# Kernel tuning notes

Hardware: AMD Instinct MI355X
Metric: run time of the kernel (lower is better)

The kernel has to match this reference:

```python
import jax, jax.numpy as jnp
import numpy as np

N = 100000      # nodes
E = 1600000     # edges
G = 256         # graphs in the batch
D_IN = 128
H = 128
C = 10
EPS = 1e-5      # BatchNorm eps


def setup_inputs() -> dict:
    key = jax.random.key(0)
    ks = jax.random.split(key, 32)
    inp = {
        'x': jax.random.normal(ks[0], (N, D_IN), jnp.float32),
        'edge_index': jax.random.randint(ks[1], (2, E), 0, N, dtype=jnp.int64),
        'batch': jnp.sort(jax.random.randint(ks[2], (N,), 0, G, dtype=jnp.int64)),
        'w1': jax.random.normal(ks[3], (D_IN, H), jnp.float32) * 0.05,
        'b1': jax.random.normal(ks[4], (H,), jnp.float32) * 0.05,
        'w2': jax.random.normal(ks[5], (H, H), jnp.float32) * 0.05,
        'b2': jax.random.normal(ks[6], (H,), jnp.float32) * 0.05,
        'w3': jax.random.normal(ks[7], (H, H), jnp.float32) * 0.05,
        'b3': jax.random.normal(ks[8], (H,), jnp.float32) * 0.05,
        'g1': jax.random.uniform(ks[9], (H,), jnp.float32, 0.5, 1.5),
        'be1': jax.random.normal(ks[10], (H,), jnp.float32) * 0.05,
        'm1': jax.random.normal(ks[11], (H,), jnp.float32) * 0.05,
        'v1': jax.random.uniform(ks[12], (H,), jnp.float32, 0.5, 1.5),
        'g2': jax.random.uniform(ks[13], (H,), jnp.float32, 0.5, 1.5),
        'be2': jax.random.normal(ks[14], (H,), jnp.float32) * 0.05,
        'm2': jax.random.normal(ks[15], (H,), jnp.float32) * 0.05,
        'v2': jax.random.uniform(ks[16], (H,), jnp.float32, 0.5, 1.5),
        'g3': jax.random.uniform(ks[17], (H,), jnp.float32, 0.5, 1.5),
        'be3': jax.random.normal(ks[18], (H,), jnp.float32) * 0.05,
        'm3': jax.random.normal(ks[19], (H,), jnp.float32) * 0.05,
        'v3': jax.random.uniform(ks[20], (H,), jnp.float32, 0.5, 1.5),
        'fcw1': jax.random.normal(ks[21], (H, H // 2), jnp.float32) * 0.05,
        'fcb1': jax.random.normal(ks[22], (H // 2,), jnp.float32) * 0.05,
        'fcw2': jax.random.normal(ks[23], (H // 2, C), jnp.float32) * 0.05,
        'fcb2': jax.random.normal(ks[24], (C,), jnp.float32) * 0.05,
    }
    return inp


def _gcn_norm(edge_index, n_nodes):
    # add self loops (PyG GCNConv default) and compute D^-1/2 (A+I) D^-1/2 norms
    loop = jnp.arange(n_nodes, dtype=edge_index.dtype)
    src = jnp.concatenate([edge_index[0], loop])
    dst = jnp.concatenate([edge_index[1], loop])
    deg = jax.ops.segment_sum(jnp.ones_like(dst, dtype=jnp.float32), dst, num_segments=n_nodes)
    dinv = jnp.where(deg > 0, jax.lax.rsqrt(deg), 0.0)
    norm = dinv[src] * dinv[dst]  # [E+N]
    return src, dst, norm


def _gcn_conv(x, W, b, src, dst, norm, n_nodes):
    h = x @ W                                   # [N, H]
    msg = norm[:, None] * h[src]                # gather + scale, [E+N, H]
    return jax.ops.segment_sum(msg, dst, num_segments=n_nodes) + b


def _bn_eval(x, gamma, beta, mean, var):
    return (x - mean) * jax.lax.rsqrt(var + EPS) * gamma + beta


def reference(x, edge_index, batch, w1, b1, w2, b2, w3, b3,
              g1, be1, m1, v1, g2, be2, m2, v2, g3, be3, m3, v3,
              fcw1, fcb1, fcw2, fcb2):
    n = x.shape[0]
    x = jnp.nan_to_num(x, nan=0.0, posinf=1e6, neginf=-1e6)
    src, dst, norm = _gcn_norm(edge_index, n)

    h = jax.nn.relu(_bn_eval(_gcn_conv(x, w1, b1, src, dst, norm, n), g1, be1, m1, v1))
    h = jax.nn.relu(_bn_eval(_gcn_conv(h, w2, b2, src, dst, norm, n), g2, be2, m2, v2))
    h = jax.nn.relu(_bn_eval(_gcn_conv(h, w3, b3, src, dst, norm, n), g3, be3, m3, v3))

    # global_mean_pool over graphs
    sums = jax.ops.segment_sum(h, batch, num_segments=G)            # [G, H]
    cnts = jax.ops.segment_sum(jnp.ones((n,), h.dtype), batch, num_segments=G)
    pooled = sums / jnp.maximum(cnts, 1.0)[:, None]

    out = jax.nn.relu(pooled @ fcw1 + fcb1) @ fcw2 + fcb2           # [G, C]
    return out
```

## Files before the change

### kernel.cpp

```cpp
#include <hip/hip_runtime.h>
#include <math.h>

#define NN 100000
#define EE 1600000
#define GG 256
#define HH 128
#define BSH 8
#define NBK 391
#define PASSA_WG 391
#define CAPB 6144

typedef __attribute__((ext_vector_type(8))) short short8;
typedef __attribute__((ext_vector_type(4))) float f32x4;

union U4S8 { uint4 u; short8 s; };

static __device__ __forceinline__ unsigned bf16rne(float f) {
    const unsigned u = __float_as_uint(f);
    return (u + 0x7fffu + ((u >> 16) & 1u)) >> 16;
}
static __device__ __forceinline__ unsigned packbf(float a, float b) {
    return bf16rne(a) | (bf16rne(b) << 16);
}
static __device__ __forceinline__ float bflo(unsigned u) { return __uint_as_float(u << 16); }
static __device__ __forceinline__ float bfhi(unsigned u) { return __uint_as_float(u & 0xffff0000u); }

__global__ void detect_k(const int* __restrict__ ei, const int* __restrict__ batch,
                         int* __restrict__ flags) {
    if (threadIdx.x == 0 && blockIdx.x == 0) {
        int e64 = 1;
        for (int j = 0; j < 8; ++j) {
            if (ei[2 * EE - 1 - 2 * j] != 0) { e64 = 0; break; }
        }
        flags[0] = e64;
        flags[1] = (batch[NN - 1] == 0) ? 1 : 0;
    }
}

__global__ __launch_bounds__(512) void cursinit_k(int* __restrict__ cursor) {
    const int b = blockIdx.x * 512 + threadIdx.x;
    if (b < NBK) cursor[b] = b * CAPB;
}

__global__ void bnprep_k(const float* __restrict__ b1, const float* __restrict__ g1,
                         const float* __restrict__ be1, const float* __restrict__ m1,
                         const float* __restrict__ v1,
                         const float* __restrict__ b2, const float* __restrict__ g2,
                         const float* __restrict__ be2, const float* __restrict__ m2,
                         const float* __restrict__ v2,
                         const float* __restrict__ b3, const float* __restrict__ g3,
                         const float* __restrict__ be3, const float* __restrict__ m3,
                         const float* __restrict__ v3,
                         float* __restrict__ sc, float* __restrict__ sh) {
    const int c = threadIdx.x;
    float s;
    s = g1[c] / sqrtf(v1[c] + 1e-5f);
    sc[c] = s;           sh[c] = (b1[c] - m1[c]) * s + be1[c];
    s = g2[c] / sqrtf(v2[c] + 1e-5f);
    sc[128 + c] = s;     sh[128 + c] = (b2[c] - m2[c]) * s + be2[c];
    s = g3[c] / sqrtf(v3[c] + 1e-5f);
    sc[256 + c] = s;     sh[256 + c] = (b3[c] - m3[c]) * s + be3[c];
}

__global__ __launch_bounds__(256) void wprep_k(const float* __restrict__ w1,
                                               const float* __restrict__ w2,
                                               const float* __restrict__ w3,
                                               unsigned* __restrict__ bt) {
    const int id = blockIdx.x * 256 + threadIdx.x;
    if (id >= 3 * 8192) return;
    const int w = id >> 13;
    const int rem = id & 8191;
    const int n = rem >> 6;
    const int kk = rem & 63;
    const float* W = (w == 0) ? w1 : (w == 1) ? w2 : w3;
    bt[id] = packbf(W[(2 * kk) * HH + n], W[(2 * kk + 1) * HH + n]);
}

__global__ __launch_bounds__(256) void passA_k(const int* __restrict__ ei,
                                               const int* __restrict__ flags,
                                               int* __restrict__ cursor,
                                               unsigned* __restrict__ pairs) {
    __shared__ int h[NBK];
    __shared__ int rbase[NBK];
    const int tid = threadIdx.x;
    for (int i = tid; i < NBK; i += 256) h[i] = 0;
    __syncthreads();
    const bool e64 = flags[0] != 0;
    const int base = blockIdx.x * 4096;
    int scache[16], dcache[16];
#pragma unroll
    for (int j = 0; j < 16; ++j) {
        const int e = base + j * 256 + tid;
        int s = -1, d = 0;
        if (e < EE) {
            s = e64 ? ei[2 * e] : ei[e];
            d = e64 ? ei[2 * (EE + e)] : ei[EE + e];
            atomicAdd(&h[d >> BSH], 1);
        }
        scache[j] = s; dcache[j] = d;
    }
    __syncthreads();
    for (int i = tid; i < NBK; i += 256) {
        const int c = h[i];
        rbase[i] = c ? atomicAdd(&cursor[i], c) : 0;
    }
    __syncthreads();
    for (int i = tid; i < NBK; i += 256) h[i] = 0;
    __syncthreads();
#pragma unroll
    for (int j = 0; j < 16; ++j) {
        const int s = scache[j];
        if (s >= 0) {
            const int d = dcache[j];
            const int b = d >> BSH;
            const int r = atomicAdd(&h[b], 1);
            pairs[rbase[b] + r] = ((unsigned)(d & 255) << 17) | (unsigned)s;
        }
    }
}

__global__ __launch_bounds__(256) void passB_k(const unsigned* __restrict__ pairs,
                                               const int* __restrict__ cursor,
                                               int* __restrict__ offs,
                                               int* __restrict__ degcnt,
                                               float* __restrict__ dinv,
                                               int* __restrict__ csr) {
    __shared__ unsigned pk[CAPB];
    __shared__ int cnt[256];
    __shared__ int loff[256];
    __shared__ int sc[256];
    const int tid = threadIdx.x;
    const int b = blockIdx.x;
    const int p0 = b * CAPB;
    const int np = cursor[b] - p0;
    const int nb0 = b << BSH;
    const int nnode = (NN - nb0 < 256) ? (NN - nb0) : 256;

    cnt[tid] = 0;
    __syncthreads();
    for (int i = tid; i < np; i += 256) {
        const unsigned p = pairs[p0 + i];
        pk[i] = p;
        atomicAdd(&cnt[p >> 17], 1);
    }
    __syncthreads();
    const int creal = cnt[tid];
    const int cpad = (tid < nnode) ? ((creal + 8) & ~7) : 0;
    sc[tid] = cpad;
    __syncthreads();
    for (int off = 1; off < 256; off <<= 1) {
        int t = (tid >= off) ? sc[tid - off] : 0;
        __syncthreads();
        sc[tid] += t;
        __syncthreads();
    }
    const int ex = sc[tid] - cpad;
    loff[tid] = ex;
    if (tid < nnode) {
        const int node = nb0 + tid;
        offs[node] = p0 + ex;
        degcnt[node] = creal;
        dinv[node] = 1.0f / sqrtf((float)(creal + 1));
    }
    __syncthreads();
    cnt[tid] = 0;
    __syncthreads();
    for (int i = tid; i < np; i += 256) {
        const unsigned p = pk[i];
        const int dl = (int)(p >> 17);
        const int r = atomicAdd(&cnt[dl], 1);
        csr[p0 + loff[dl] + r] = (int)(p & 0x1FFFFu);
    }
    if (tid < nnode) {
        const int basep = p0 + loff[tid];
        csr[basep + creal] = nb0 + tid;
        for (int j = creal + 1; j < cpad; ++j) csr[basep + j] = NN;
    }
}

static __device__ __forceinline__ float sani(float v) {
    if (isnan(v)) return 0.0f;
    if (isinf(v)) return v > 0.0f ? 1e6f : -1e6f;
    return v;
}

template <bool AF32>
__global__ __launch_bounds__(256) void gemm_mfma_k(const float* __restrict__ Af,
                                                   const unsigned* __restrict__ Abf,
                                                   const unsigned* __restrict__ btg,
                                                   const float* __restrict__ dinv,
                                                   unsigned* __restrict__ C, int M) {
    __shared__ unsigned lds_u[8704];
    const int tid = threadIdx.x;
    const int wave = tid >> 6;
    const int lane = tid & 63;
    const int nl = lane & 15;
    const int q = lane >> 4;
    const int row0 = blockIdx.x * 64 + wave * 16;
    const int rowg = row0 + nl;
    const int rowa = min(rowg, M - 1);

    {
        const uint4* __restrict__ bg4 = (const uint4*)btg;
        for (int i = tid; i < 2048; i += 256) {
            const int n = i >> 4, w4 = i & 15;
            *(uint4*)&lds_u[n * 68 + w4 * 4] = bg4[n * 16 + w4];
        }
    }

    short8 a[4];
    if (AF32) {
#pragma unroll
        for (int ks = 0; ks < 4; ++ks) {
            const float4 p = *(const float4*)(Af + (size_t)rowa * HH + ks * 32 + q * 8);
            const float4 r = *(const float4*)(Af + (size_t)rowa * HH + ks * 32 + q * 8 + 4);
            U4S8 cv;
            cv.u = make_uint4(packbf(sani(p.x), sani(p.y)), packbf(sani(p.z), sani(p.w)),
                              packbf(sani(r.x), sani(r.y)), packbf(sani(r.z), sani(r.w)));
            a[ks] = cv.s;
        }
    } else {
#pragma unroll
        for (int ks = 0; ks < 4; ++ks) {
            U4S8 cv;
            cv.u = *(const uint4*)(Abf + (size_t)rowa * 64 + ks * 16 + q * 4);
            a[ks] = cv.s;
        }
    }

    __syncthreads();

    f32x4 acc[8];
#pragma unroll
    for (int t = 0; t < 8; ++t) acc[t] = (f32x4)0.0f;

    const unsigned short* __restrict__ bts = (const unsigned short*)lds_u;
#pragma unroll
    for (int ks = 0; ks < 4; ++ks) {
#pragma unroll
        for (int t = 0; t < 8; ++t) {
            const int n = t * 16 + nl;
            const short8 b = *(const short8*)(bts + n * 136 + ks * 32 + q * 8);
            acc[t] = __builtin_amdgcn_mfma_f32_16x16x32_bf16(b, a[ks], acc[t], 0, 0, 0);
        }
    }

    if (rowg < M) {
        const float dsc = dinv[rowg];
        unsigned* crow = C + (size_t)rowg * 64;
#pragma unroll
        for (int t = 0; t < 8; ++t) {
            uint2 o;
            o.x = packbf(dsc * acc[t][0], dsc * acc[t][1]);
            o.y = packbf(dsc * acc[t][2], dsc * acc[t][3]);
            *(uint2*)(crow + t * 8 + q * 2) = o;
        }
    } else if (rowg == M) {
        unsigned* crow = C + (size_t)M * 64;
#pragma unroll
        for (int t = 0; t < 8; ++t)
            *(uint2*)(crow + t * 8 + q * 2) = make_uint2(0u, 0u);
    }
}

__global__ __launch_bounds__(256) void aggregate_k(
    const unsigned* __restrict__ hpre, const int* __restrict__ csr,
    const int* __restrict__ offs, const int* __restrict__ cnt,
    const float* __restrict__ dinv,
    const float* __restrict__ bnsc, const float* __restrict__ bnsh,
    unsigned* __restrict__ xout) {
    const int v = __builtin_amdgcn_readfirstlane(blockIdx.x * 4 + (threadIdx.x >> 6));
    const int lane = threadIdx.x & 63;
    const int cg = lane & 15;
    const int sub = lane >> 4;
    const int c8 = cg * 8;

    const float dv = dinv[v];
    const int start = offs[v];
    const int npad = (cnt[v] + 8) & ~7;
    const char* __restrict__ hb = (const char*)hpre;
    const unsigned cgo = (unsigned)(cg << 4);

    float acc[8];
#pragma unroll
    for (int j = 0; j < 8; ++j) acc[j] = 0.0f;

    int i = 0;
    for (; i + 16 <= npad; i += 16) {
        const int sA = csr[start + i + sub];
        const int sB = csr[start + i + 4 + sub];
        const int sC = csr[start + i + 8 + sub];
        const int sD = csr[start + i + 12 + sub];
        const uint4 rA = *(const uint4*)(hb + (((unsigned)sA << 8) | cgo));
        const uint4 rB = *(const uint4*)(hb + (((unsigned)sB << 8) | cgo));
        const uint4 rC = *(const uint4*)(hb + (((unsigned)sC << 8) | cgo));
        const uint4 rD = *(const uint4*)(hb + (((unsigned)sD << 8) | cgo));
        acc[0] += (bflo(rA.x) + bflo(rB.x)) + (bflo(rC.x) + bflo(rD.x));
        acc[1] += (bfhi(rA.x) + bfhi(rB.x)) + (bfhi(rC.x) + bfhi(rD.x));
        acc[2] += (bflo(rA.y) + bflo(rB.y)) + (bflo(rC.y) + bflo(rD.y));
        acc[3] += (bfhi(rA.y) + bfhi(rB.y)) + (bfhi(rC.y) + bfhi(rD.y));
        acc[4] += (bflo(rA.z) + bflo(rB.z)) + (bflo(rC.z) + bflo(rD.z));
        acc[5] += (bfhi(rA.z) + bfhi(rB.z)) + (bfhi(rC.z) + bfhi(rD.z));
        acc[6] += (bflo(rA.w) + bflo(rB.w)) + (bflo(rC.w) + bflo(rD.w));
        acc[7] += (bfhi(rA.w) + bfhi(rB.w)) + (bfhi(rC.w) + bfhi(rD.w));
    }
    if (i < npad) {
        const int sA = csr[start + i + sub];
        const int sB = csr[start + i + 4 + sub];
        const uint4 rA = *(const uint4*)(hb + (((unsigned)sA << 8) | cgo));
        const uint4 rB = *(const uint4*)(hb + (((unsigned)sB << 8) | cgo));
        acc[0] += bflo(rA.x) + bflo(rB.x);
        acc[1] += bfhi(rA.x) + bfhi(rB.x);
        acc[2] += bflo(rA.y) + bflo(rB.y);
        acc[3] += bfhi(rA.y) + bfhi(rB.y);
        acc[4] += bflo(rA.z) + bflo(rB.z);
        acc[5] += bfhi(rA.z) + bfhi(rB.z);
        acc[6] += bflo(rA.w) + bflo(rB.w);
        acc[7] += bfhi(rA.w) + bfhi(rB.w);
    }

#pragma unroll
    for (int j = 0; j < 8; ++j) {
        acc[j] += __shfl_xor(acc[j], 16);
        acc[j] += __shfl_xor(acc[j], 32);
    }

    if (sub == 0) {
        const float4 sca = *(const float4*)(bnsc + c8);
        const float4 scb = *(const float4*)(bnsc + c8 + 4);
        const float4 sha = *(const float4*)(bnsh + c8);
        const float4 shb = *(const float4*)(bnsh + c8 + 4);
        const float y0 = fmaxf(dv * acc[0] * sca.x + sha.x, 0.0f);
        const float y1 = fmaxf(dv * acc[1] * sca.y + sha.y, 0.0f);
        const float y2 = fmaxf(dv * acc[2] * sca.z + sha.z, 0.0f);
        const float y3 = fmaxf(dv * acc[3] * sca.w + sha.w, 0.0f);
        const float y4 = fmaxf(dv * acc[4] * scb.x + shb.x, 0.0f);
        const float y5 = fmaxf(dv * acc[5] * scb.y + shb.y, 0.0f);
        const float y6 = fmaxf(dv * acc[6] * scb.z + shb.z, 0.0f);
        const float y7 = fmaxf(dv * acc[7] * scb.w + shb.w, 0.0f);
        *(uint4*)(xout + (size_t)v * 64 + cg * 4) =
            make_uint4(packbf(y0, y1), packbf(y2, y3), packbf(y4, y5), packbf(y6, y7));
    }
}

__global__ __launch_bounds__(256) void pool_sum_k(
    const unsigned* __restrict__ x, const int* __restrict__ batch,
    const int* __restrict__ flags, float* __restrict__ psum,
    int* __restrict__ gcnt) {
    const int wave = threadIdx.x >> 6;
    const int lane = threadIdx.x & 63;
    const int row0 = blockIdx.x * 64 + wave * 16;
    if (row0 >= NN) return;
    const bool b64 = flags[1] != 0;

    float sx = 0.0f, sy = 0.0f;
    int cur = -1, runlen = 0;
#pragma unroll
    for (int r = 0; r < 16; ++r) {
        const int row = row0 + r;
        if (row >= NN) break;
        const int g = b64 ? batch[2 * row] : batch[row];
        if (g != cur) {
            if (cur >= 0) {
                atomicAdd(&psum[cur * HH + lane * 2 + 0], sx);
                atomicAdd(&psum[cur * HH + lane * 2 + 1], sy);
                if (lane == 0) atomicAdd(&gcnt[cur], runlen);
            }
            cur = g; sx = 0.0f; sy = 0.0f; runlen = 0;
        }
        const unsigned u = x[(size_t)row * 64 + lane];
        sx += bflo(u);
        sy += bfhi(u);
        ++runlen;
    }
    if (cur >= 0) {
        atomicAdd(&psum[cur * HH + lane * 2 + 0], sx);
        atomicAdd(&psum[cur * HH + lane * 2 + 1], sy);
        if (lane == 0) atomicAdd(&gcnt[cur], runlen);
    }
}

__global__ __launch_bounds__(128) void head_k(
    const float* __restrict__ psum, const int* __restrict__ gcnt,
    const float* __restrict__ fw1, const float* __restrict__ fb1,
    const float* __restrict__ fw2, const float* __restrict__ fb2,
    float* __restrict__ out) {
    __shared__ float pooled[128];
    __shared__ float hid[64];
    const int g = blockIdx.x;
    const int tid = threadIdx.x;

    const int cntn = gcnt[g];
    pooled[tid] = psum[g * HH + tid] / (float)(cntn > 0 ? cntn : 1);
    __syncthreads();

    if (tid < 64) {
        float a = fb1[tid];
#pragma unroll 4
        for (int k = 0; k < 128; ++k) a += pooled[k] * fw1[k * 64 + tid];
        hid[tid] = fmaxf(a, 0.0f);
    }
    __syncthreads();
    if (tid < 10) {
        float a = fb2[tid];
#pragma unroll
        for (int k = 0; k < 64; ++k) a += hid[k] * fw2[k * 10 + tid];
        out[g * 10 + tid] = a;
    }
}

extern "C" void kernel_launch(void* const* d_in, const int* in_sizes, int n_in,
                              void* d_out, int out_size, void* d_ws, size_t ws_size,
                              hipStream_t stream) {
    const float* x_in  = (const float*)d_in[0];
    const int*   ei    = (const int*)d_in[1];
    const int*   batch = (const int*)d_in[2];
    const float* w1 = (const float*)d_in[3];
    const float* b1 = (const float*)d_in[4];
    const float* w2 = (const float*)d_in[5];
    const float* b2 = (const float*)d_in[6];
    const float* w3 = (const float*)d_in[7];
    const float* b3 = (const float*)d_in[8];
    const float* g1 = (const float*)d_in[9];
    const float* be1 = (const float*)d_in[10];
    const float* m1 = (const float*)d_in[11];
    const float* v1 = (const float*)d_in[12];
    const float* g2 = (const float*)d_in[13];
    const float* be2 = (const float*)d_in[14];
    const float* m2 = (const float*)d_in[15];
    const float* v2 = (const float*)d_in[16];
    const float* g3 = (const float*)d_in[17];
    const float* be3 = (const float*)d_in[18];
    const float* m3 = (const float*)d_in[19];
    const float* v3 = (const float*)d_in[20];
    const float* fw1 = (const float*)d_in[21];
    const float* fb1 = (const float*)d_in[22];
    const float* fw2 = (const float*)d_in[23];
    const float* fb2 = (const float*)d_in[24];
    float* out = (float*)d_out;

    size_t off = 0;
    char* base = (char*)d_ws;
    auto alloc = [&](size_t bytes) -> void* {
        void* p = base + off;
        off += (bytes + 255) & ~(size_t)255;
        return p;
    };
    int*      degcnt = (int*)alloc((size_t)NN * 4);
    float*    dinv   = (float*)alloc((size_t)NN * 4);
    int*      offs   = (int*)alloc((size_t)NN * 4);
    int*      cursor = (int*)alloc((size_t)NBK * 4);
    int*      flags  = (int*)alloc(256);
    float*    bnsc   = (float*)alloc(3 * 128 * 4);
    float*    bnsh   = (float*)alloc(3 * 128 * 4);
    unsigned* btg    = (unsigned*)alloc(3 * 8192 * 4);
    float*    psum   = (float*)alloc((size_t)GG * HH * 4);
    int*      gcnt   = (int*)alloc((size_t)GG * 4);
    int*      csr    = (int*)alloc((size_t)NBK * CAPB * 4);
    unsigned* pairs  = (unsigned*)alloc((size_t)NBK * CAPB * 4);
    unsigned* bufx   = (unsigned*)alloc((size_t)NN * 64 * 4);
    unsigned* hpre   = (unsigned*)alloc((size_t)(NN + 1) * 64 * 4);
    if (off > ws_size) return;

    detect_k<<<1, 64, 0, stream>>>(ei, batch, flags);
    cursinit_k<<<1, 512, 0, stream>>>(cursor);
    bnprep_k<<<1, 128, 0, stream>>>(b1, g1, be1, m1, v1,
                                    b2, g2, be2, m2, v2,
                                    b3, g3, be3, m3, v3, bnsc, bnsh);
    wprep_k<<<96, 256, 0, stream>>>(w1, w2, w3, btg);
    hipMemsetAsync(psum, 0, (size_t)GG * HH * 4, stream);
    hipMemsetAsync(gcnt, 0, (size_t)GG * 4, stream);
    passA_k<<<PASSA_WG, 256, 0, stream>>>(ei, flags, cursor, pairs);
    passB_k<<<NBK, 256, 0, stream>>>(pairs, cursor, offs, degcnt, dinv, csr);

    const int ggrid = (NN + 63) / 64;
    const int agrid = NN / 4;

    gemm_mfma_k<true><<<ggrid, 256, 0, stream>>>(x_in, nullptr, btg, dinv, hpre, NN);
    aggregate_k<<<agrid, 256, 0, stream>>>(hpre, csr, offs, degcnt, dinv,
                                           bnsc, bnsh, bufx);
    gemm_mfma_k<false><<<ggrid, 256, 0, stream>>>(nullptr, bufx, btg + 8192, dinv, hpre, NN);
    aggregate_k<<<agrid, 256, 0, stream>>>(hpre, csr, offs, degcnt, dinv,
                                           bnsc + 128, bnsh + 128, bufx);
    gemm_mfma_k<false><<<ggrid, 256, 0, stream>>>(nullptr, bufx, btg + 16384, dinv, hpre, NN);
    aggregate_k<<<agrid, 256, 0, stream>>>(hpre, csr, offs, degcnt, dinv,
                                           bnsc + 256, bnsh + 256, bufx);

    pool_sum_k<<<ggrid, 256, 0, stream>>>(bufx, batch, flags, psum, gcnt);
    head_k<<<GG, 128, 0, stream>>>(psum, gcnt, fw1, fb1, fw2, fb2, out);
}
```

Baseline: 446.0 us.

## Fuse setup kernels and memsets into one launch; shrink passA edge chunk

Four small setup kernels (edge-dtype detection, cursor init, BN fold, weight bf16 pack) and two memsets are merged into a single setup kernel that partitions its thread IDs across the tasks, cutting launch and inter-kernel gaps. Separately, passA now processes 1024 edges per workgroup with 1563 workgroups instead of 4096 edges across 391, which spreads the bucketing pass over more CUs. The trade-off is more global cursor atomics and smaller, less coalesced per-bucket runs in the pairs buffer.

Measured after the change: 463.0 us. 1.04x slower.

```diff
diff --git a/kernel.cpp b/kernel.cpp
--- a/kernel.cpp
+++ b/kernel.cpp
@@ -7,7 +7,7 @@
 #define HH 128
 #define BSH 8
 #define NBK 391
-#define PASSA_WG 391
+#define PASSA_WG 1563
 #define CAPB 6144
 
 typedef __attribute__((ext_vector_type(8))) short short8;
@@ -25,9 +25,47 @@
 static __device__ __forceinline__ float bflo(unsigned u) { return __uint_as_float(u << 16); }
 static __device__ __forceinline__ float bfhi(unsigned u) { return __uint_as_float(u & 0xffff0000u); }
 
-__global__ void detect_k(const int* __restrict__ ei, const int* __restrict__ batch,
-                         int* __restrict__ flags) {
-    if (threadIdx.x == 0 && blockIdx.x == 0) {
+__global__ __launch_bounds__(256) void setup_k(
+    const int* __restrict__ ei, const int* __restrict__ batch,
+    const float* __restrict__ w1, const float* __restrict__ w2,
+    const float* __restrict__ w3,
+    const float* __restrict__ b1, const float* __restrict__ g1,
+    const float* __restrict__ be1, const float* __restrict__ m1,
+    const float* __restrict__ v1,
+    const float* __restrict__ b2, const float* __restrict__ g2,
+    const float* __restrict__ be2, const float* __restrict__ m2,
+    const float* __restrict__ v2,
+    const float* __restrict__ b3, const float* __restrict__ g3,
+    const float* __restrict__ be3, const float* __restrict__ m3,
+    const float* __restrict__ v3,
+    unsigned* __restrict__ bt, float* __restrict__ sc, float* __restrict__ sh,
+    int* __restrict__ cursor, float* __restrict__ psum, int* __restrict__ gcnt,
+    int* __restrict__ flags) {
+    const int id = blockIdx.x * 256 + threadIdx.x;
+    if (id < 24576) {
+        const int w = id >> 13;
+        const int rem = id & 8191;
+        const int n = rem >> 6;
+        const int kk = rem & 63;
+        const float* W = (w == 0) ? w1 : (w == 1) ? w2 : w3;
+        bt[id] = packbf(W[(2 * kk) * HH + n], W[(2 * kk + 1) * HH + n]);
+    } else if (id < 24704) {
+        const int c = id - 24576;
+        float s;
+        s = g1[c] / sqrtf(v1[c] + 1e-5f);
+        sc[c] = s;           sh[c] = (b1[c] - m1[c]) * s + be1[c];
+        s = g2[c] / sqrtf(v2[c] + 1e-5f);
+        sc[128 + c] = s;     sh[128 + c] = (b2[c] - m2[c]) * s + be2[c];
+        s = g3[c] / sqrtf(v3[c] + 1e-5f);
+        sc[256 + c] = s;     sh[256 + c] = (b3[c] - m3[c]) * s + be3[c];
+    } else if (id < 25095) {
+        const int b = id - 24704;
+        cursor[b] = b * CAPB;
+    } else if (id < 57863) {
+        psum[id - 25095] = 0.0f;
+    } else if (id < 58119) {
+        gcnt[id - 57863] = 0;
+    } else if (id == 58119) {
         int e64 = 1;
         for (int j = 0; j < 8; ++j) {
             if (ei[2 * EE - 1 - 2 * j] != 0) { e64 = 0; break; }
@@ -36,45 +74,7 @@
         flags[1] = (batch[NN - 1] == 0) ? 1 : 0;
     }
 }
-
-__global__ __launch_bounds__(512) void cursinit_k(int* __restrict__ cursor) {
-    const int b = blockIdx.x * 512 + threadIdx.x;
-    if (b < NBK) cursor[b] = b * CAPB;
-}
-
-__global__ void bnprep_k(const float* __restrict__ b1, const float* __restrict__ g1,
-                         const float* __restrict__ be1, const float* __restrict__ m1,
-                         const float* __restrict__ v1,
-                         const float* __restrict__ b2, const float* __restrict__ g2,
-                         const float* __restrict__ be2, const float* __restrict__ m2,
-                         const float* __restrict__ v2,
-                         const float* __restrict__ b3, const float* __restrict__ g3,
-                         const float* __restrict__ be3, const float* __restrict__ m3,
-                         const float* __restrict__ v3,
-                         float* __restrict__ sc, float* __restrict__ sh) {
-    const int c = threadIdx.x;
-    float s;
-    s = g1[c] / sqrtf(v1[c] + 1e-5f);
-    sc[c] = s;           sh[c] = (b1[c] - m1[c]) * s + be1[c];
-    s = g2[c] / sqrtf(v2[c] + 1e-5f);
-    sc[128 + c] = s;     sh[128 + c] = (b2[c] - m2[c]) * s + be2[c];
-    s = g3[c] / sqrtf(v3[c] + 1e-5f);
-    sc[256 + c] = s;     sh[256 + c] = (b3[c] - m3[c]) * s + be3[c];
-}
-
-__global__ __launch_bounds__(256) void wprep_k(const float* __restrict__ w1,
-                                               const float* __restrict__ w2,
-                                               const float* __restrict__ w3,
-                                               unsigned* __restrict__ bt) {
-    const int id = blockIdx.x * 256 + threadIdx.x;
-    if (id >= 3 * 8192) return;
-    const int w = id >> 13;
-    const int rem = id & 8191;
-    const int n = rem >> 6;
-    const int kk = rem & 63;
-    const float* W = (w == 0) ? w1 : (w == 1) ? w2 : w3;
-    bt[id] = packbf(W[(2 * kk) * HH + n], W[(2 * kk + 1) * HH + n]);
-}
+#define SETUP_GRID 228
 
 __global__ __launch_bounds__(256) void passA_k(const int* __restrict__ ei,
                                                const int* __restrict__ flags,
@@ -86,10 +86,10 @@
     for (int i = tid; i < NBK; i += 256) h[i] = 0;
     __syncthreads();
     const bool e64 = flags[0] != 0;
-    const int base = blockIdx.x * 4096;
-    int scache[16], dcache[16];
-#pragma unroll
-    for (int j = 0; j < 16; ++j) {
+    const int base = blockIdx.x * 1024;
+    int scache[4], dcache[4];
+#pragma unroll
+    for (int j = 0; j < 4; ++j) {
         const int e = base + j * 256 + tid;
         int s = -1, d = 0;
         if (e < EE) {
@@ -108,7 +108,7 @@
     for (int i = tid; i < NBK; i += 256) h[i] = 0;
     __syncthreads();
 #pragma unroll
-    for (int j = 0; j < 16; ++j) {
+    for (int j = 0; j < 4; ++j) {
         const int s = scache[j];
         if (s >= 0) {
             const int d = dcache[j];
@@ -462,14 +462,12 @@
     unsigned* hpre   = (unsigned*)alloc((size_t)(NN + 1) * 64 * 4);
     if (off > ws_size) return;
 
-    detect_k<<<1, 64, 0, stream>>>(ei, batch, flags);
-    cursinit_k<<<1, 512, 0, stream>>>(cursor);
-    bnprep_k<<<1, 128, 0, stream>>>(b1, g1, be1, m1, v1,
-                                    b2, g2, be2, m2, v2,
-                                    b3, g3, be3, m3, v3, bnsc, bnsh);
-    wprep_k<<<96, 256, 0, stream>>>(w1, w2, w3, btg);
-    hipMemsetAsync(psum, 0, (size_t)GG * HH * 4, stream);
-    hipMemsetAsync(gcnt, 0, (size_t)GG * 4, stream);
+    setup_k<<<SETUP_GRID, 256, 0, stream>>>(ei, batch, w1, w2, w3,
+                                            b1, g1, be1, m1, v1,
+                                            b2, g2, be2, m2, v2,
+                                            b3, g3, be3, m3, v3,
+                                            btg, bnsc, bnsh, cursor, psum, gcnt,
+                                            flags);
     passA_k<<<PASSA_WG, 256, 0, stream>>>(ei, flags, cursor, pairs);
     passB_k<<<NBK, 256, 0, stream>>>(pairs, cursor, offs, degcnt, dinv, csr);
 
```
